# Kernel optimization log

Measured on AMD Instinct MI355X. Metric: run time of the kernel, lower is better.

## Reference

```python
import jax, jax.numpy as jnp
import numpy as np
from jax import lax

B, C, H, W = 2, 64, 128, 128
NBR, G, K, P, CK = 4, 8, 3, 11, 3
PAD = 6  # (CK-1)//2 + (P-1)//2


def conv2d(x, w, b, pad):
    y = lax.conv_general_dilated(x, w, (1, 1), [(pad, pad), (pad, pad)],
                                 dimension_numbers=('NCHW', 'OIHW', 'NCHW'))
    return y + b[None, :, None, None]


def l2norm(x):
    n = jnp.sqrt(jnp.sum(x * x, axis=1, keepdims=True))
    return x / jnp.maximum(n, 1e-12)


def correlation(f1, f2):
    # spatial correlation sampler: kernel=3, patch=11, stride=1, padding=1
    # corr[b, ph*11+pw, h, w] = sum_{c,ki,kj} f1[b,c,h+ki-1,w+kj-1]*f2[b,c,h+ki-1+ph-5,w+kj-1+pw-5]
    f1p = jnp.pad(f1, ((0, 0), (0, 0), (1, 1), (1, 1)))
    f2p = jnp.pad(f2, ((0, 0), (0, 0), (PAD, PAD), (PAD, PAD)))
    offs = jnp.array([(ph, pw) for ph in range(P) for pw in range(P)], dtype=jnp.int32)

    def one(off):
        sl = lax.dynamic_slice(f2p, (0, 0, off[0], off[1]), (B, C, H + 2, W + 2))
        q = jnp.einsum('bchw,bchw->bhw', f1p, sl)  # (B,H+2,W+2)
        # 3x3 box sum -> (B,H,W)
        return sum(q[:, ki:ki + H, kj:kj + W] for ki in range(CK) for kj in range(CK))

    corr = lax.map(one, offs)  # (121,B,H,W)
    return jnp.transpose(corr, (1, 0, 2, 3))  # (B,121,H,W)


def setup_inputs() -> dict:
    key = jax.random.key(0)
    ks = jax.random.split(key, 12)
    s = 0.05
    return {
        'nbr_fea': jax.random.normal(ks[0], (B, C, H, W), jnp.float32),
        'ref_fea': jax.random.normal(ks[1], (B, C, H, W), jnp.float32),
        'conv1_w': jax.random.normal(ks[2], (C, 2 * C, 3, 3), jnp.float32) * s,
        'conv1_b': jax.random.normal(ks[3], (C,), jnp.float32) * s,
        'conv2_w': jax.random.normal(ks[4], (C, C, 3, 3), jnp.float32) * s,
        'conv2_b': jax.random.normal(ks[5], (C,), jnp.float32) * s,
        'mask_w': jax.random.normal(ks[6], (G * K * K, C, K, K), jnp.float32) * s,
        'mask_b': jax.random.normal(ks[7], (G * K * K,), jnp.float32) * s,
        'nn_w': jax.random.normal(ks[8], (C, NBR * C, 3, 3), jnp.float32) * s,
        'nn_b': jax.random.normal(ks[9], (C,), jnp.float32) * s,
        'agg_w': jax.random.normal(ks[10], (C, 2 * C, 3, 3), jnp.float32) * s,
        'agg_b': jax.random.normal(ks[11], (C,), jnp.float32) * s,
    }


def reference(nbr_fea, ref_fea, conv1_w, conv1_b, conv2_w, conv2_b,
              mask_w, mask_b, nn_w, nn_b, agg_w, agg_b):
    # mask branch
    wf = conv2d(jnp.concatenate([nbr_fea, ref_fea], axis=1), conv1_w, conv1_b, 1)
    wf = conv2d(wf, conv2_w, conv2_b, 1)
    mask = conv2d(wf, mask_w, mask_b, (K - 1) // 2).reshape(B, G, 1, K * K, H, W)

    # local correlation + topk neighbor selection
    corr = correlation(l2norm(ref_fea), l2norm(nbr_fea))  # (B,121,H,W)
    idx = lax.top_k(jnp.transpose(corr, (0, 2, 3, 1)), NBR)[1]  # (B,H,W,NBR)
    ph, pw = idx // P, idx % P

    # gather 3x3 patches centered at displacement (ph-5, pw-5) from pad-6 nbr features
    nbr_pad = jnp.pad(nbr_fea, ((0, 0), (0, 0), (PAD, PAD), (PAD, PAD)))
    r0 = jnp.arange(H)[None, :, None, None] + ph  # (B,H,W,NBR) top-left row in padded img
    c0 = jnp.arange(W)[None, None, :, None] + pw
    ki = jnp.arange(CK)

    def gather_b(fp, r, c):
        R = r[..., None, None] + ki[:, None]   # (H,W,NBR,3,1)
        Cc = c[..., None, None] + ki[None, :]  # (H,W,NBR,1,3)
        return fp[:, R, Cc]  # (C,H,W,NBR,3,3)

    patches = jax.vmap(gather_b)(nbr_pad, r0, c0)  # (B,C,H,W,NBR,3,3)
    L = jnp.transpose(patches, (0, 2, 3, 4, 1, 5, 6)).reshape(B * H * W, NBR * C, CK, CK)
    L = conv2d(L, nn_w, nn_b, 1)  # (B*H*W, C, 3, 3)
    L = L.reshape(B, H, W, C, CK * CK)
    L = jnp.transpose(L, (0, 3, 4, 1, 2)).reshape(B, G, C // G, CK * CK, H, W)

    agg = jnp.sum(L * mask, axis=3).reshape(B, C, H, W)
    agg = jnp.where(agg >= 0, agg, 0.1 * agg)  # LeakyReLU(0.1)
    out = conv2d(jnp.concatenate([agg, ref_fea], axis=1), agg_w, agg_b, 1)
    return out
```

## Files before the change

kernel.cpp:

```cpp
#include <hip/hip_runtime.h>
#include <hip/hip_bf16.h>
#include <math.h>

#define HH 128
#define WW 128
#define HWSZ 16384

typedef __attribute__((ext_vector_type(8))) short short8;
typedef __attribute__((ext_vector_type(4))) float f32x4;

constexpr int OFF_CATT  = 0;
constexpr int OFF_CAT2T = 8388608;
constexpr int OFF_WF1   = 16777216;
constexpr int OFF_WF2   = 20971520;
constexpr int OFF_MASK  = 25165824;
constexpr int OFF_IDX   = 34603008;
constexpr int OFF_WT1   = 35127296;
constexpr int OFF_WT2   = 35274752;
constexpr int OFF_WTM   = 35348480;
constexpr int OFF_WTA   = 35495936;
constexpr int OFF_ZROW  = 35643392;
constexpr int OFF_WB    = 35644416;
constexpr int OFF_F1T   = 38797312;
constexpr int OFF_F2T   = 47185920;
constexpr int OFF_D     = 55574528;
constexpr int OFF_PV    = 71434240;
constexpr int OFF_PP    = 77201408;

__device__ inline ushort f2bf(float f) {
    __hip_bfloat16 h = __float2bfloat16(f);
    return *reinterpret_cast<ushort*>(&h);
}
__device__ inline float bf2f(ushort u) {
    return __uint_as_float(((unsigned)u) << 16);
}

__device__ inline void gload16(const void* g, void* l) {
    __builtin_amdgcn_global_load_lds(
        (const __attribute__((address_space(1))) unsigned int*)g,
        (__attribute__((address_space(3))) unsigned int*)l, 16, 0, 0);
}

__global__ __launch_bounds__(256) void l2t2_kernel(const float* __restrict__ in,
                                                   float4* __restrict__ normT4,
                                                   ushort* __restrict__ d1,
                                                   ushort* __restrict__ d2)
{
    const int pix0 = blockIdx.x * 64;
    const int b = pix0 >> 14;
    const int hw0 = pix0 & (HWSZ - 1);
    __shared__ float s[64][65];
    __shared__ float sinv[64];
    const int tid = threadIdx.x;
    {
        const int p = tid & 63, c4 = tid >> 6;
#pragma unroll
        for (int r = 0; r < 16; ++r) {
            int c = r * 4 + c4;
            s[c][p] = in[(((size_t)b * 64 + c) << 14) + hw0 + p];
        }
    }
    __syncthreads();
    if (tid < 64) {
        float sum = 0.f;
#pragma unroll
        for (int c = 0; c < 64; ++c) { float v = s[c][tid]; sum = fmaf(v, v, sum); }
        sinv[tid] = 1.f / fmaxf(sqrtf(sum), 1e-12f);
    }
    __syncthreads();
    {
        const int pp = tid & 63, cg = tid >> 6;
        const float inv = sinv[pp];
#pragma unroll
        for (int r = 0; r < 4; ++r) {
            int c4 = cg * 4 + r;
            float4 v = make_float4(s[c4 * 4 + 0][pp] * inv, s[c4 * 4 + 1][pp] * inv,
                                   s[c4 * 4 + 2][pp] * inv, s[c4 * 4 + 3][pp] * inv);
            normT4[(((size_t)b * 16 + c4) << 14) + hw0 + pp] = v;
        }
    }
    {
        const int c = tid & 63, p4 = tid >> 6;
#pragma unroll
        for (int r = 0; r < 16; ++r) {
            int pp = r * 4 + p4;
            ushort bv = f2bf(s[c][pp]);
            d1[(size_t)(pix0 + pp) * 128 + c] = bv;
            if (d2) d2[(size_t)(pix0 + pp) * 128 + c] = bv;
        }
    }
}

__global__ __launch_bounds__(256) void dot_kernel(const float4* __restrict__ f1t4,
                                                  const float4* __restrict__ f2t4,
                                                  float* __restrict__ D)
{
    const int pix = blockIdx.x * 256 + threadIdx.x;
    const int q = blockIdx.y;
    const int b = pix >> 14, hw = pix & (HWSZ - 1), h = hw >> 7, w = hw & 127;
    const int y = h + q - 5;
    float* Dq = D + ((((size_t)b * 121) + q * 11) << 14) + hw;

    if ((unsigned)y >= (unsigned)HH) {
#pragma unroll
        for (int pw = 0; pw < 11; ++pw) Dq[(size_t)pw << 14] = 0.f;
        return;
    }
    float acc[11] = {};
    const float4* f1p  = f1t4 + (((size_t)b * 16) << 14) + hw;
    const float4* rowb = f2t4 + (((size_t)b * 16) << 14) + (y << 7);

#pragma unroll 4
    for (int c4 = 0; c4 < 16; ++c4) {
        float4 a = f1p[(size_t)c4 << 14];
        const float4* rp = rowb + ((size_t)c4 << 14);
#pragma unroll
        for (int pw = 0; pw < 11; ++pw) {
            int x = w + pw - 5;
            if ((unsigned)x < (unsigned)WW) {
                float4 c = rp[x];
                acc[pw] = fmaf(a.x, c.x, acc[pw]);
                acc[pw] = fmaf(a.y, c.y, acc[pw]);
                acc[pw] = fmaf(a.z, c.z, acc[pw]);
                acc[pw] = fmaf(a.w, c.w, acc[pw]);
            }
        }
    }
#pragma unroll
    for (int pw = 0; pw < 11; ++pw) Dq[(size_t)pw << 14] = acc[pw];
}

__global__ __launch_bounds__(256) void topk_s1(const float* __restrict__ D,
                                               float4* __restrict__ Pv,
                                               int4* __restrict__ Pp)
{
    const int pix = blockIdx.x * 256 + threadIdx.x;
    const int q = blockIdx.y;
    const int b = pix >> 14, hw = pix & (HWSZ - 1), h = hw >> 7, w = hw & 127;
    const int lane = threadIdx.x & 63;
    const float* Db = D + (((size_t)b * 121) << 14);

    float bv[4] = {-1e30f, -1e30f, -1e30f, -1e30f};
    int   bi[4] = {1 << 20, 1 << 20, 1 << 20, 1 << 20};

    for (int pw = 0; pw < 11; ++pw) {
        const int p = q * 11 + pw;
        const float* Dp = Db + ((size_t)p << 14);
        float v = 0.f, vx = 0.f;
#pragma unroll
        for (int dy = -1; dy <= 1; ++dy) {
            int y = h + dy;
            if ((unsigned)y < HH) {
                v += Dp[(y << 7) + w];
                if (lane == 0) { if (w > 0) vx += Dp[(y << 7) + w - 1]; }
                else if (lane == 63) { if (w < 127) vx += Dp[(y << 7) + w + 1]; }
            }
        }
        float vl = __shfl_up(v, 1);
        float vr = __shfl_down(v, 1);
        if (lane == 0)  vl = (w > 0)   ? vx : 0.f;
        if (lane == 63) vr = (w < 127) ? vx : 0.f;
        float s = vl + v + vr;
        if (s > bv[3]) {
            if (s > bv[0]) { bv[3]=bv[2];bi[3]=bi[2]; bv[2]=bv[1];bi[2]=bi[1]; bv[1]=bv[0];bi[1]=bi[0]; bv[0]=s; bi[0]=p; }
            else if (s > bv[1]) { bv[3]=bv[2];bi[3]=bi[2]; bv[2]=bv[1];bi[2]=bi[1]; bv[1]=s; bi[1]=p; }
            else if (s > bv[2]) { bv[3]=bv[2];bi[3]=bi[2]; bv[2]=s; bi[2]=p; }
            else { bv[3]=s; bi[3]=p; }
        }
    }
    Pv[(size_t)q * 32768 + pix] = make_float4(bv[0], bv[1], bv[2], bv[3]);
    Pp[(size_t)q * 32768 + pix] = make_int4(bi[0], bi[1], bi[2], bi[3]);
}

__global__ __launch_bounds__(256) void topk_s2(const float4* __restrict__ Pv,
                                               const int4* __restrict__ Pp,
                                               int* __restrict__ idxout)
{
    const int pix = blockIdx.x * 256 + threadIdx.x;
    float bv2[4] = {-1e30f, -1e30f, -1e30f, -1e30f};
    int   bi2[4] = {1 << 20, 1 << 20, 1 << 20, 1 << 20};
    for (int qq = 0; qq < 11; ++qq) {
        float4 v4 = Pv[(size_t)qq * 32768 + pix];
        int4   p4 = Pp[(size_t)qq * 32768 + pix];
        float vv[4] = {v4.x, v4.y, v4.z, v4.w};
        int   pp4[4] = {p4.x, p4.y, p4.z, p4.w};
#pragma unroll
        for (int r = 0; r < 4; ++r) {
            float v = vv[r]; int pp = pp4[r];
            bool g3 = (v > bv2[3]) || (v == bv2[3] && pp < bi2[3]);
            if (g3) {
                bool g0 = (v > bv2[0]) || (v == bv2[0] && pp < bi2[0]);
                bool g1 = (v > bv2[1]) || (v == bv2[1] && pp < bi2[1]);
                bool g2 = (v > bv2[2]) || (v == bv2[2] && pp < bi2[2]);
                if (g0) { bv2[3]=bv2[2];bi2[3]=bi2[2]; bv2[2]=bv2[1];bi2[2]=bi2[1]; bv2[1]=bv2[0];bi2[1]=bi2[0]; bv2[0]=v; bi2[0]=pp; }
                else if (g1) { bv2[3]=bv2[2];bi2[3]=bi2[2]; bv2[2]=bv2[1];bi2[2]=bi2[1]; bv2[1]=v; bi2[1]=pp; }
                else if (g2) { bv2[3]=bv2[2];bi2[3]=bi2[2]; bv2[2]=v; bi2[2]=pp; }
                else { bv2[3]=v; bi2[3]=pp; }
            }
        }
    }
    int p0 = (bi2[0] / 11) | ((bi2[0] % 11) << 16);
    int p1 = (bi2[1] / 11) | ((bi2[1] % 11) << 16);
    int p2 = (bi2[2] / 11) | ((bi2[2] % 11) << 16);
    int p3 = (bi2[3] / 11) | ((bi2[3] % 11) << 16);
    ((int4*)idxout)[pix] = make_int4(p0, p1, p2, p3);
}

__device__ inline ushort wt_elem(const float* __restrict__ w, int Cin, int Cout, int idx) {
    int kc = 9 * Cin;
    int o = idx / kc, rem = idx % kc;
    int tap = rem / Cin, c = rem % Cin;
    float val = (o < Cout) ? w[((size_t)o * Cin + c) * 9 + tap] : 0.f;
    return f2bf(val);
}

__global__ __launch_bounds__(256) void prep_kernel(
    const float* __restrict__ c1w, const float* __restrict__ c2w,
    const float* __restrict__ mw,  const float* __restrict__ aw,
    const float* __restrict__ nnw, char* __restrict__ W)
{
    int gid = blockIdx.x * 256 + threadIdx.x;
    if (gid < 73728) {
        ((ushort*)(W + OFF_WT1))[gid] = wt_elem(c1w, 128, 64, gid);
    } else if (gid < 110592) {
        int i = gid - 73728;
        ((ushort*)(W + OFF_WT2))[i] = wt_elem(c2w, 64, 64, i);
    } else if (gid < 165888) {
        int i = gid - 110592;
        ((ushort*)(W + OFF_WTM))[i] = wt_elem(mw, 64, 72, i);
    } else if (gid < 239616) {
        int i = gid - 165888;
        ((ushort*)(W + OFF_WTA))[i] = wt_elem(aw, 128, 64, i);
    } else if (gid < 387072) {
        int idx = gid - 239616;
        int j = idx / 36864, rem = idx % 36864;
        int rb = rem >> 6, c = rem & 63;
        int e = rb >> 6, o = rb & 63;
        int ky = e / 3, kx = e % 3;
        ((ushort*)(W + OFF_WB))[idx] =
            f2bf(nnw[(((size_t)o * 256 + j * 64 + c) * 3 + ky) * 3 + kx]);
    } else if (gid < 387200) {
        ((ushort*)(W + OFF_ZROW))[gid - 387072] = 0;
    }
}

template<int CINPT, int OUTFMT, int BM, int BN, int WN>
__global__ __launch_bounds__(256) void mmconv_kernel(
    const char* __restrict__ Wb, int src_off, int rowbytes, int zoff,
    const ushort* __restrict__ WT, int Ktot,
    const float* __restrict__ bias,
    void* __restrict__ outp, int ostride, int nvalid)
{
    constexpr int WM = 4 / WN;
    constexpr int FM = BM / (WM * 16);
    constexpr int FN = BN / (WN * 16);
    constexpr int NA = BM / 32;
    constexpr int NB = BN / 32;
    const int n0 = blockIdx.x * BN;
    const int m0 = blockIdx.y * BM;
    const int tid = threadIdx.x;
    const int lane = tid & 63, wv = tid >> 6;
    const int lr = lane >> 4, lc = lane & 15;
    const int wr = wv / WN, wc = wv % WN;

    __shared__ __align__(16) char sA[2][BM * 128];
    __shared__ __align__(16) char sB[2][BN * 128];

    int hA[NA], wA[NA], aBase[NA], swzA[NA];
#pragma unroll
    for (int i = 0; i < NA; ++i) {
        int r  = (i * 4 + wv) * 8 + (lane >> 3);
        int pm = m0 + r;
        int hw = pm & (HWSZ - 1);
        hA[i] = hw >> 7; wA[i] = hw & 127;
        aBase[i] = src_off + (pm >> 14) * (HWSZ * rowbytes);
        swzA[i]  = ((lane & 7) ^ (r & 7)) << 4;
    }
    int boff[NB];
#pragma unroll
    for (int i = 0; i < NB; ++i) {
        int rb = (i * 4 + wv) * 8 + (lane >> 3);
        boff[i] = (n0 + rb) * Ktot * 2 + (((lane & 7) ^ (rb & 7)) << 4);
    }

    f32x4 acc[FM][FN] = {};
    const int NST = Ktot / 64;

#define CSTAGE(S, B)                                                             \
    {                                                                            \
        int k0 = (S) * 64;                                                       \
        int tap = k0 / CINPT;                                                    \
        int c0b = (k0 % CINPT) * 2;                                              \
        int du = tap / 3 - 1, dv = tap % 3 - 1;                                  \
        _Pragma("unroll")                                                        \
        for (int i = 0; i < NA; ++i) {                                           \
            int y = hA[i] + du, x = wA[i] + dv;                                  \
            bool ok = ((unsigned)y < (unsigned)HH) && ((unsigned)x < (unsigned)WW); \
            int off = ok ? (aBase[i] + ((y << 7) + x) * rowbytes + c0b + swzA[i]) : zoff; \
            gload16(Wb + (unsigned)off, &sA[(B)][(i * 4 + wv) * 1024]);          \
        }                                                                        \
        _Pragma("unroll")                                                        \
        for (int i = 0; i < NB; ++i)                                             \
            gload16((const char*)WT + (unsigned)(boff[i] + (S) * 128),           \
                    &sB[(B)][(i * 4 + wv) * 1024]);                              \
    }

    CSTAGE(0, 0)
    __syncthreads();
#pragma unroll 1
    for (int s = 0; s < NST; ++s) {
        if (s + 1 < NST) { CSTAGE(s + 1, (s + 1) & 1) }
        const char* cA = sA[s & 1];
        const char* cB = sB[s & 1];
#pragma unroll
        for (int ks = 0; ks < 2; ++ks) {
            short8 af[FM]; short8 bfr[FN];
            const int u = ks * 4 + lr;
#pragma unroll
            for (int f = 0; f < FM; ++f) {
                int rr = wr * (FM * 16) + f * 16 + lc;
                af[f] = *(const short8*)&cA[rr * 128 + ((u ^ (rr & 7)) << 4)];
            }
#pragma unroll
            for (int g = 0; g < FN; ++g) {
                int nn = wc * (FN * 16) + g * 16 + lc;
                bfr[g] = *(const short8*)&cB[nn * 128 + ((u ^ (nn & 7)) << 4)];
            }
#pragma unroll
            for (int f = 0; f < FM; ++f)
#pragma unroll
                for (int g = 0; g < FN; ++g)
                    acc[f][g] = __builtin_amdgcn_mfma_f32_16x16x32_bf16(af[f], bfr[g], acc[f][g], 0, 0, 0);
        }
        __syncthreads();
    }
#undef CSTAGE

#pragma unroll
    for (int f = 0; f < FM; ++f)
#pragma unroll
        for (int g = 0; g < FN; ++g) {
            const int col = n0 + wc * (FN * 16) + g * 16 + lc;
            float bv = (bias != nullptr && col < nvalid) ? bias[col] : 0.f;
            if (OUTFMT == 2) {
                const int mb = m0 + wr * (FM * 16) + f * 16 + lr * 4;
                const int bb = mb >> 14, hww = mb & (HWSZ - 1);
                float4 o4 = {acc[f][g][0] + bv, acc[f][g][1] + bv,
                             acc[f][g][2] + bv, acc[f][g][3] + bv};
                *(float4*)((float*)outp + (((size_t)(bb * 64 + col)) << 14) + hww) = o4;
            } else {
#pragma unroll
                for (int reg = 0; reg < 4; ++reg) {
                    const int m = m0 + wr * (FM * 16) + f * 16 + lr * 4 + reg;
                    float v = acc[f][g][reg] + bv;
                    if (OUTFMT == 0)
                        ((ushort*)outp)[(size_t)m * ostride + col] = f2bf(v);
                    else if (col < nvalid)
                        ((float*)outp)[(size_t)m * ostride + col] = v;
                }
            }
        }
}

__global__ __launch_bounds__(256, 2) void patch_kernel(
    const char* __restrict__ Wb, int cat_off, int idx_off, int zoff, int wb_off,
    const float* __restrict__ maskcl, const float* __restrict__ nnb,
    ushort* __restrict__ aggout)
{
    const int m0 = blockIdx.x * 32;
    const int tid = threadIdx.x;
    const int lane = tid & 63, wv = tid >> 6;
    const int lr = lane >> 4, lc = lane & 15;
    const int wr = wv >> 1, wc = wv & 1;

    __shared__ __align__(16) char sP[36864 + 2 * 16384];

    const int r    = tid >> 3;
    const int pm_s = m0 + r;
    const int hw_s = pm_s & (HWSZ - 1);
    const int hS = hw_s >> 7, wS = hw_s & 127;
    const int aBase = cat_off + (pm_s >> 14) * (HWSZ * 256);
    const int swzA  = ((tid & 7) ^ (r & 7)) << 4;
    int bsrc[2];
#pragma unroll
    for (int i = 0; i < 2; ++i) {
        int rl = i * 32 + r;
        bsrc[i] = wb_off + rl * 128 + (((tid & 7) ^ (rl & 7)) << 4);
    }
    const int* idxr = (const int*)(Wb + idx_off);

    f32x4 acc[9][2] = {};

#pragma unroll 1
    for (int j = 0; j < 4; ++j) {
        const int pk = idxr[pm_s * 4 + j];
        const int hp = hS + (pk & 0xffff) - 6;
        const int wp = wS + (pk >> 16) - 6;

        __syncthreads();
#pragma unroll
        for (int uv = 0; uv < 9; ++uv) {
            int y = hp + uv / 3, x = wp + uv % 3;
            bool ok = ((unsigned)y < (unsigned)HH) && ((unsigned)x < (unsigned)WW);
            int off = ok ? (aBase + ((y << 7) + x) * 256 + swzA) : zoff;
            gload16(Wb + (unsigned)off, &sP[uv * 4096 + wv * 1024]);
        }
#pragma unroll
        for (int eg = 0; eg < 2; ++eg)
#pragma unroll
            for (int i = 0; i < 2; ++i)
                gload16(Wb + (unsigned)(bsrc[i] + j * 73728 + eg * 8192),
                        &sP[36864 + eg * 8192 + i * 4096 + wv * 1024]);
        __syncthreads();

        short8 af[9][2];
#pragma unroll
        for (int uv = 0; uv < 9; ++uv)
#pragma unroll
            for (int ks = 0; ks < 2; ++ks) {
                const int rr = wr * 16 + lc;
                af[uv][ks] = *(const short8*)&sP[uv * 4096 + rr * 128 +
                                                (((ks * 4 + lr) ^ (rr & 7)) << 4)];
            }

#pragma unroll
        for (int g = 0; g < 5; ++g) {
            if (g < 4) {
                const int nslot = (g + 1) & 1;
#pragma unroll
                for (int eg = 0; eg < 2; ++eg) {
                    const int ne = 2 * (g + 1) + eg;
                    if (ne > 8) continue;
#pragma unroll
                    for (int i = 0; i < 2; ++i)
                        gload16(Wb + (unsigned)(bsrc[i] + j * 73728 + ne * 8192),
                                &sP[36864 + nslot * 16384 + eg * 8192 + i * 4096 + wv * 1024]);
                }
            }
#pragma unroll
            for (int eg = 0; eg < 2; ++eg) {
                const int e = 2 * g + eg;
                if (e > 8) continue;
                const char* bt = &sP[36864 + (g & 1) * 16384 + eg * 8192];
                short8 bfr[2][2];
#pragma unroll
                for (int gg = 0; gg < 2; ++gg) {
                    const int rloc = wc * 32 + gg * 16 + lc;
#pragma unroll
                    for (int ks = 0; ks < 2; ++ks)
                        bfr[gg][ks] = *(const short8*)&bt[rloc * 128 +
                                                          (((ks * 4 + lr) ^ (rloc & 7)) << 4)];
                }
                const int ky = e / 3, kx = e % 3;
#pragma unroll
                for (int uv = 0; uv < 9; ++uv) {
                    const int uu = uv / 3, vv = uv % 3;
                    const int ty = uu - ky + 1, tx = vv - kx + 1;
                    if (ty < 0 || ty > 2 || tx < 0 || tx > 2) continue;
                    const int t = ty * 3 + tx;
#pragma unroll
                    for (int gg = 0; gg < 2; ++gg) {
                        acc[t][gg] = __builtin_amdgcn_mfma_f32_16x16x32_bf16(af[uv][0], bfr[gg][0], acc[t][gg], 0, 0, 0);
                        acc[t][gg] = __builtin_amdgcn_mfma_f32_16x16x32_bf16(af[uv][1], bfr[gg][1], acc[t][gg], 0, 0, 0);
                    }
                }
            }
            if (g < 4) __syncthreads();
        }
    }

#pragma unroll
    for (int gg = 0; gg < 2; ++gg) {
        const int col_o = wc * 32 + gg * 16 + lc;
        const float bo = nnb[col_o];
        const int og = col_o >> 3;
#pragma unroll
        for (int reg = 0; reg < 4; ++reg) {
            const int m = m0 + wr * 16 + lr * 4 + reg;
            const float* mp = maskcl + (size_t)m * 72 + og * 9;
            float s = 0.f;
#pragma unroll
            for (int t = 0; t < 9; ++t) s += (acc[t][gg][reg] + bo) * mp[t];
            s = (s >= 0.f) ? s : 0.1f * s;
            aggout[(size_t)m * 128 + col_o] = f2bf(s);
        }
    }
}

extern "C" void kernel_launch(void* const* d_in, const int* in_sizes, int n_in,
                              void* d_out, int out_size, void* d_ws, size_t ws_size,
                              hipStream_t stream)
{
    const float* nbr = (const float*)d_in[0];
    const float* ref = (const float*)d_in[1];
    const float* c1w = (const float*)d_in[2];
    const float* c1b = (const float*)d_in[3];
    const float* c2w = (const float*)d_in[4];
    const float* c2b = (const float*)d_in[5];
    const float* mw  = (const float*)d_in[6];
    const float* mb  = (const float*)d_in[7];
    const float* nnw = (const float*)d_in[8];
    const float* nnb = (const float*)d_in[9];
    const float* aw  = (const float*)d_in[10];
    const float* ab  = (const float*)d_in[11];
    float* out = (float*)d_out;

    char* W = (char*)d_ws;
    float4* f1t4   = (float4*)(W + OFF_F1T);
    float4* f2t4   = (float4*)(W + OFF_F2T);
    float*  Dbuf   = (float*)(W + OFF_D);
    float*  maskcl = (float*)(W + OFF_MASK);
    int*    idxp   = (int*)(W + OFF_IDX);
    ushort* catT   = (ushort*)(W + OFF_CATT);
    ushort* cat2T  = (ushort*)(W + OFF_CAT2T);

    dim3 blk(256);

    prep_kernel<<<1513, blk, 0, stream>>>(c1w, c2w, mw, aw, nnw, W);

    l2t2_kernel<<<512, blk, 0, stream>>>(ref, f1t4, catT + 64, cat2T + 64);
    l2t2_kernel<<<512, blk, 0, stream>>>(nbr, f2t4, catT + 0, (ushort*)nullptr);

    mmconv_kernel<128, 0, 32, 64, 4><<<dim3(1, 1024), blk, 0, stream>>>(
        W, OFF_CATT, 256, OFF_ZROW, (ushort*)(W + OFF_WT1), 1152, c1b, W + OFF_WF1, 64, 64);
    mmconv_kernel<64, 0, 32, 64, 4><<<dim3(1, 1024), blk, 0, stream>>>(
        W, OFF_WF1, 128, OFF_ZROW, (ushort*)(W + OFF_WT2), 576, c2b, W + OFF_WF2, 64, 64);
    mmconv_kernel<64, 1, 32, 96, 2><<<dim3(1, 1024), blk, 0, stream>>>(
        W, OFF_WF2, 128, OFF_ZROW, (ushort*)(W + OFF_WTM), 576, mb, maskcl, 72, 72);

    dot_kernel<<<dim3(128, 11), blk, 0, stream>>>(f1t4, f2t4, Dbuf);
    topk_s1<<<dim3(128, 11), blk, 0, stream>>>(Dbuf, (float4*)(W + OFF_PV), (int4*)(W + OFF_PP));
    topk_s2<<<128, blk, 0, stream>>>((const float4*)(W + OFF_PV), (const int4*)(W + OFF_PP), idxp);

    patch_kernel<<<1024, blk, 0, stream>>>(W, OFF_CATT, OFF_IDX, OFF_ZROW, OFF_WB,
                                           maskcl, nnb, cat2T);

    mmconv_kernel<128, 2, 32, 64, 4><<<dim3(1, 1024), blk, 0, stream>>>(
        W, OFF_CAT2T, 256, OFF_ZROW, (ushort*)(W + OFF_WTA), 1152, ab, out, 0, 64);
}
```

Baseline: 177.8 us.

## Fuse correlation dot product with 3x3 box-sum top-k stage via LDS

Merges the per-offset dot-product kernel and the first top-k stage into one kernel that keeps the raw dot products for a tile of rows in shared memory, then box-sums and selects the top 4 per row of offsets. This removes the full-size global D buffer write and reread plus one launch. In exchange each block recomputes two halo rows, uses 56KB of LDS, and the grid shrinks to 352 blocks, which lowers occupancy and parallelism.

```diff
diff --git a/kernel.cpp b/kernel.cpp
--- a/kernel.cpp
+++ b/kernel.cpp
@@ -23,9 +23,8 @@
 constexpr int OFF_WB    = 35644416;
 constexpr int OFF_F1T   = 38797312;
 constexpr int OFF_F2T   = 47185920;
-constexpr int OFF_D     = 55574528;
-constexpr int OFF_PV    = 71434240;
-constexpr int OFF_PP    = 77201408;
+constexpr int OFF_PV    = 55574528;
+constexpr int OFF_PP    = 61341696;
 
 __device__ inline ushort f2bf(float f) {
     __hip_bfloat16 h = __float2bfloat16(f);
@@ -91,85 +90,80 @@
     }
 }
 
-__global__ __launch_bounds__(256) void dot_kernel(const float4* __restrict__ f1t4,
-                                                  const float4* __restrict__ f2t4,
-                                                  float* __restrict__ D)
-{
-    const int pix = blockIdx.x * 256 + threadIdx.x;
+__global__ __launch_bounds__(256) void corr_kernel(const float4* __restrict__ f1t4,
+                                                   const float4* __restrict__ f2t4,
+                                                   float4* __restrict__ Pv,
+                                                   int4* __restrict__ Pp)
+{
     const int q = blockIdx.y;
-    const int b = pix >> 14, hw = pix & (HWSZ - 1), h = hw >> 7, w = hw & 127;
-    const int y = h + q - 5;
-    float* Dq = D + ((((size_t)b * 121) + q * 11) << 14) + hw;
-
-    if ((unsigned)y >= (unsigned)HH) {
-#pragma unroll
-        for (int pw = 0; pw < 11; ++pw) Dq[(size_t)pw << 14] = 0.f;
-        return;
-    }
-    float acc[11] = {};
-    const float4* f1p  = f1t4 + (((size_t)b * 16) << 14) + hw;
-    const float4* rowb = f2t4 + (((size_t)b * 16) << 14) + (y << 7);
-
+    const int b = blockIdx.x >> 4;
+    const int brow0 = (blockIdx.x & 15) * 8;
+    const int tid = threadIdx.x;
+
+    __shared__ float Dl[10][11][128];
+
+    const size_t fbase = ((size_t)b * 16) << 14;
+
+#pragma unroll 1
+    for (int k = 0; k < 5; ++k) {
+        const int task = tid + k * 256;
+        const int trow = task >> 7;
+        const int w = task & 127;
+        const int rg = brow0 + trow - 1;
+        const int y = rg + q - 5;
+        float acc[11] = {};
+        if ((unsigned)rg < (unsigned)HH && (unsigned)y < (unsigned)HH) {
+            const float4* f1p  = f1t4 + fbase + (rg << 7) + w;
+            const float4* rowb = f2t4 + fbase + (y << 7);
 #pragma unroll 4
-    for (int c4 = 0; c4 < 16; ++c4) {
-        float4 a = f1p[(size_t)c4 << 14];
-        const float4* rp = rowb + ((size_t)c4 << 14);
+            for (int c4 = 0; c4 < 16; ++c4) {
+                float4 a = f1p[(size_t)c4 << 14];
+                const float4* rp = rowb + ((size_t)c4 << 14);
+#pragma unroll
+                for (int pw = 0; pw < 11; ++pw) {
+                    int x = w + pw - 5;
+                    if ((unsigned)x < (unsigned)WW) {
+                        float4 c = rp[x];
+                        acc[pw] = fmaf(a.x, c.x, acc[pw]);
+                        acc[pw] = fmaf(a.y, c.y, acc[pw]);
+                        acc[pw] = fmaf(a.z, c.z, acc[pw]);
+                        acc[pw] = fmaf(a.w, c.w, acc[pw]);
+                    }
+                }
+            }
+        }
+#pragma unroll
+        for (int pw = 0; pw < 11; ++pw) Dl[trow][pw][w] = acc[pw];
+    }
+    __syncthreads();
+
+#pragma unroll 1
+    for (int k = 0; k < 4; ++k) {
+        const int opix = tid + k * 256;
+        const int orow = opix >> 7;
+        const int w = opix & 127;
+        float bv[4] = {-1e30f, -1e30f, -1e30f, -1e30f};
+        int   bi[4] = {1 << 20, 1 << 20, 1 << 20, 1 << 20};
 #pragma unroll
         for (int pw = 0; pw < 11; ++pw) {
-            int x = w + pw - 5;
-            if ((unsigned)x < (unsigned)WW) {
-                float4 c = rp[x];
-                acc[pw] = fmaf(a.x, c.x, acc[pw]);
-                acc[pw] = fmaf(a.y, c.y, acc[pw]);
-                acc[pw] = fmaf(a.z, c.z, acc[pw]);
-                acc[pw] = fmaf(a.w, c.w, acc[pw]);
-            }
-        }
-    }
-#pragma unroll
-    for (int pw = 0; pw < 11; ++pw) Dq[(size_t)pw << 14] = acc[pw];
-}
-
-__global__ __launch_bounds__(256) void topk_s1(const float* __restrict__ D,
-                                               float4* __restrict__ Pv,
-                                               int4* __restrict__ Pp)
-{
-    const int pix = blockIdx.x * 256 + threadIdx.x;
-    const int q = blockIdx.y;
-    const int b = pix >> 14, hw = pix & (HWSZ - 1), h = hw >> 7, w = hw & 127;
-    const int lane = threadIdx.x & 63;
-    const float* Db = D + (((size_t)b * 121) << 14);
-
-    float bv[4] = {-1e30f, -1e30f, -1e30f, -1e30f};
-    int   bi[4] = {1 << 20, 1 << 20, 1 << 20, 1 << 20};
-
-    for (int pw = 0; pw < 11; ++pw) {
-        const int p = q * 11 + pw;
-        const float* Dp = Db + ((size_t)p << 14);
-        float v = 0.f, vx = 0.f;
-#pragma unroll
-        for (int dy = -1; dy <= 1; ++dy) {
-            int y = h + dy;
-            if ((unsigned)y < HH) {
-                v += Dp[(y << 7) + w];
-                if (lane == 0) { if (w > 0) vx += Dp[(y << 7) + w - 1]; }
-                else if (lane == 63) { if (w < 127) vx += Dp[(y << 7) + w + 1]; }
-            }
-        }
-        float vl = __shfl_up(v, 1);
-        float vr = __shfl_down(v, 1);
-        if (lane == 0)  vl = (w > 0)   ? vx : 0.f;
-        if (lane == 63) vr = (w < 127) ? vx : 0.f;
-        float s = vl + v + vr;
-        if (s > bv[3]) {
-            if (s > bv[0]) { bv[3]=bv[2];bi[3]=bi[2]; bv[2]=bv[1];bi[2]=bi[1]; bv[1]=bv[0];bi[1]=bi[0]; bv[0]=s; bi[0]=p; }
-            else if (s > bv[1]) { bv[3]=bv[2];bi[3]=bi[2]; bv[2]=bv[1];bi[2]=bi[1]; bv[1]=s; bi[1]=p; }
-            else if (s > bv[2]) { bv[3]=bv[2];bi[3]=bi[2]; bv[2]=s; bi[2]=p; }
-            else { bv[3]=s; bi[3]=p; }
-        }
-    }
-    Pv[(size_t)q * 32768 + pix] = make_float4(bv[0], bv[1], bv[2], bv[3]);
-    Pp[(size_t)q * 32768 + pix] = make_int4(bi[0], bi[1], bi[2], bi[3]);
+            const int p = q * 11 + pw;
+            float v  = Dl[orow][pw][w] + Dl[orow + 1][pw][w] + Dl[orow + 2][pw][w];
+            float vl = (w > 0)
+                ? Dl[orow][pw][w - 1] + Dl[orow + 1][pw][w - 1] + Dl[orow + 2][pw][w - 1] : 0.f;
+            float vr = (w < 127)
+                ? Dl[orow][pw][w + 1] + Dl[orow + 1][pw][w + 1] + Dl[orow + 2][pw][w + 1] : 0.f;
+            float s = vl + v + vr;
+            if (s > bv[3]) {
+                if (s > bv[0]) { bv[3]=bv[2];bi[3]=bi[2]; bv[2]=bv[1];bi[2]=bi[1]; bv[1]=bv[0];bi[1]=bi[0]; bv[0]=s; bi[0]=p; }
+                else if (s > bv[1]) { bv[3]=bv[2];bi[3]=bi[2]; bv[2]=bv[1];bi[2]=bi[1]; bv[1]=s; bi[1]=p; }
+                else if (s > bv[2]) { bv[3]=bv[2];bi[3]=bi[2]; bv[2]=s; bi[2]=p; }
+                else { bv[3]=s; bi[3]=p; }
+            }
+        }
+        const int pix = (b << 14) + ((brow0 + orow) << 7) + w;
+        Pv[(size_t)q * 32768 + pix] = make_float4(bv[0], bv[1], bv[2], bv[3]);
+        Pp[(size_t)q * 32768 + pix] = make_int4(bi[0], bi[1], bi[2], bi[3]);
+    }
 }
 
 __global__ __launch_bounds__(256) void topk_s2(const float4* __restrict__ Pv,
@@ -508,7 +502,6 @@
     char* W = (char*)d_ws;
     float4* f1t4   = (float4*)(W + OFF_F1T);
     float4* f2t4   = (float4*)(W + OFF_F2T);
-    float*  Dbuf   = (float*)(W + OFF_D);
     float*  maskcl = (float*)(W + OFF_MASK);
     int*    idxp   = (int*)(W + OFF_IDX);
     ushort* catT   = (ushort*)(W + OFF_CATT);
@@ -528,8 +521,8 @@
     mmconv_kernel<64, 1, 32, 96, 2><<<dim3(1, 1024), blk, 0, stream>>>(
         W, OFF_WF2, 128, OFF_ZROW, (ushort*)(W + OFF_WTM), 576, mb, maskcl, 72, 72);
 
-    dot_kernel<<<dim3(128, 11), blk, 0, stream>>>(f1t4, f2t4, Dbuf);
-    topk_s1<<<dim3(128, 11), blk, 0, stream>>>(Dbuf, (float4*)(W + OFF_PV), (int4*)(W + OFF_PP));
+    corr_kernel<<<dim3(32, 11), blk, 0, stream>>>(f1t4, f2t4,
+                                                  (float4*)(W + OFF_PV), (int4*)(W + OFF_PP));
     topk_s2<<<128, blk, 0, stream>>>((const float4*)(W + OFF_PV), (const int4*)(W + OFF_PP), idxp);
 
     patch_kernel<<<1024, blk, 0, stream>>>(W, OFF_CATT, OFF_IDX, OFF_ZROW, OFF_WB,
```

Result: slower. 236.4 us (+32.9%).

## Merge independent kernels into combined launches via block-index dispatch

Applied to the files above, without the earlier changes.

Converts the separate kernels into device bodies and builds four combined launches. Each launch pairs independent work by block index: prep with both l2-normalise passes, conv1 with the correlation dot, conv2 with topk stage one, and the mask conv with topk stage two. The aim is fewer launches and less idle time between small kernels, letting the correlation branch overlap with the conv chain. The cost is that each merged kernel's register and shared-memory footprint is the maximum of its two bodies, which may lower occupancy for the lighter half.

```diff
diff --git a/kernel.cpp b/kernel.cpp
--- a/kernel.cpp
+++ b/kernel.cpp
@@ -41,12 +41,11 @@
         (__attribute__((address_space(3))) unsigned int*)l, 16, 0, 0);
 }
 
-__global__ __launch_bounds__(256) void l2t2_kernel(const float* __restrict__ in,
-                                                   float4* __restrict__ normT4,
-                                                   ushort* __restrict__ d1,
-                                                   ushort* __restrict__ d2)
-{
-    const int pix0 = blockIdx.x * 64;
+__device__ void l2t2_body(int bid, const float* __restrict__ in,
+                          float4* __restrict__ normT4,
+                          ushort* __restrict__ d1, ushort* __restrict__ d2)
+{
+    const int pix0 = bid * 64;
     const int b = pix0 >> 14;
     const int hw0 = pix0 & (HWSZ - 1);
     __shared__ float s[64][65];
@@ -91,121 +90,6 @@
     }
 }
 
-__global__ __launch_bounds__(256) void dot_kernel(const float4* __restrict__ f1t4,
-                                                  const float4* __restrict__ f2t4,
-                                                  float* __restrict__ D)
-{
-    const int pix = blockIdx.x * 256 + threadIdx.x;
-    const int q = blockIdx.y;
-    const int b = pix >> 14, hw = pix & (HWSZ - 1), h = hw >> 7, w = hw & 127;
-    const int y = h + q - 5;
-    float* Dq = D + ((((size_t)b * 121) + q * 11) << 14) + hw;
-
-    if ((unsigned)y >= (unsigned)HH) {
-#pragma unroll
-        for (int pw = 0; pw < 11; ++pw) Dq[(size_t)pw << 14] = 0.f;
-        return;
-    }
-    float acc[11] = {};
-    const float4* f1p  = f1t4 + (((size_t)b * 16) << 14) + hw;
-    const float4* rowb = f2t4 + (((size_t)b * 16) << 14) + (y << 7);
-
-#pragma unroll 4
-    for (int c4 = 0; c4 < 16; ++c4) {
-        float4 a = f1p[(size_t)c4 << 14];
-        const float4* rp = rowb + ((size_t)c4 << 14);
-#pragma unroll
-        for (int pw = 0; pw < 11; ++pw) {
-            int x = w + pw - 5;
-            if ((unsigned)x < (unsigned)WW) {
-                float4 c = rp[x];
-                acc[pw] = fmaf(a.x, c.x, acc[pw]);
-                acc[pw] = fmaf(a.y, c.y, acc[pw]);
-                acc[pw] = fmaf(a.z, c.z, acc[pw]);
-                acc[pw] = fmaf(a.w, c.w, acc[pw]);
-            }
-        }
-    }
-#pragma unroll
-    for (int pw = 0; pw < 11; ++pw) Dq[(size_t)pw << 14] = acc[pw];
-}
-
-__global__ __launch_bounds__(256) void topk_s1(const float* __restrict__ D,
-                                               float4* __restrict__ Pv,
-                                               int4* __restrict__ Pp)
-{
-    const int pix = blockIdx.x * 256 + threadIdx.x;
-    const int q = blockIdx.y;
-    const int b = pix >> 14, hw = pix & (HWSZ - 1), h = hw >> 7, w = hw & 127;
-    const int lane = threadIdx.x & 63;
-    const float* Db = D + (((size_t)b * 121) << 14);
-
-    float bv[4] = {-1e30f, -1e30f, -1e30f, -1e30f};
-    int   bi[4] = {1 << 20, 1 << 20, 1 << 20, 1 << 20};
-
-    for (int pw = 0; pw < 11; ++pw) {
-        const int p = q * 11 + pw;
-        const float* Dp = Db + ((size_t)p << 14);
-        float v = 0.f, vx = 0.f;
-#pragma unroll
-        for (int dy = -1; dy <= 1; ++dy) {
-            int y = h + dy;
-            if ((unsigned)y < HH) {
-                v += Dp[(y << 7) + w];
-                if (lane == 0) { if (w > 0) vx += Dp[(y << 7) + w - 1]; }
-                else if (lane == 63) { if (w < 127) vx += Dp[(y << 7) + w + 1]; }
-            }
-        }
-        float vl = __shfl_up(v, 1);
-        float vr = __shfl_down(v, 1);
-        if (lane == 0)  vl = (w > 0)   ? vx : 0.f;
-        if (lane == 63) vr = (w < 127) ? vx : 0.f;
-        float s = vl + v + vr;
-        if (s > bv[3]) {
-            if (s > bv[0]) { bv[3]=bv[2];bi[3]=bi[2]; bv[2]=bv[1];bi[2]=bi[1]; bv[1]=bv[0];bi[1]=bi[0]; bv[0]=s; bi[0]=p; }
-            else if (s > bv[1]) { bv[3]=bv[2];bi[3]=bi[2]; bv[2]=bv[1];bi[2]=bi[1]; bv[1]=s; bi[1]=p; }
-            else if (s > bv[2]) { bv[3]=bv[2];bi[3]=bi[2]; bv[2]=s; bi[2]=p; }
-            else { bv[3]=s; bi[3]=p; }
-        }
-    }
-    Pv[(size_t)q * 32768 + pix] = make_float4(bv[0], bv[1], bv[2], bv[3]);
-    Pp[(size_t)q * 32768 + pix] = make_int4(bi[0], bi[1], bi[2], bi[3]);
-}
-
-__global__ __launch_bounds__(256) void topk_s2(const float4* __restrict__ Pv,
-                                               const int4* __restrict__ Pp,
-                                               int* __restrict__ idxout)
-{
-    const int pix = blockIdx.x * 256 + threadIdx.x;
-    float bv2[4] = {-1e30f, -1e30f, -1e30f, -1e30f};
-    int   bi2[4] = {1 << 20, 1 << 20, 1 << 20, 1 << 20};
-    for (int qq = 0; qq < 11; ++qq) {
-        float4 v4 = Pv[(size_t)qq * 32768 + pix];
-        int4   p4 = Pp[(size_t)qq * 32768 + pix];
-        float vv[4] = {v4.x, v4.y, v4.z, v4.w};
-        int   pp4[4] = {p4.x, p4.y, p4.z, p4.w};
-#pragma unroll
-        for (int r = 0; r < 4; ++r) {
-            float v = vv[r]; int pp = pp4[r];
-            bool g3 = (v > bv2[3]) || (v == bv2[3] && pp < bi2[3]);
-            if (g3) {
-                bool g0 = (v > bv2[0]) || (v == bv2[0] && pp < bi2[0]);
-                bool g1 = (v > bv2[1]) || (v == bv2[1] && pp < bi2[1]);
-                bool g2 = (v > bv2[2]) || (v == bv2[2] && pp < bi2[2]);
-                if (g0) { bv2[3]=bv2[2];bi2[3]=bi2[2]; bv2[2]=bv2[1];bi2[2]=bi2[1]; bv2[1]=bv2[0];bi2[1]=bi2[0]; bv2[0]=v; bi2[0]=pp; }
-                else if (g1) { bv2[3]=bv2[2];bi2[3]=bi2[2]; bv2[2]=bv2[1];bi2[2]=bi2[1]; bv2[1]=v; bi2[1]=pp; }
-                else if (g2) { bv2[3]=bv2[2];bi2[3]=bi2[2]; bv2[2]=v; bi2[2]=pp; }
-                else { bv2[3]=v; bi2[3]=pp; }
-            }
-        }
-    }
-    int p0 = (bi2[0] / 11) | ((bi2[0] % 11) << 16);
-    int p1 = (bi2[1] / 11) | ((bi2[1] % 11) << 16);
-    int p2 = (bi2[2] / 11) | ((bi2[2] % 11) << 16);
-    int p3 = (bi2[3] / 11) | ((bi2[3] % 11) << 16);
-    ((int4*)idxout)[pix] = make_int4(p0, p1, p2, p3);
-}
-
 __device__ inline ushort wt_elem(const float* __restrict__ w, int Cin, int Cout, int idx) {
     int kc = 9 * Cin;
     int o = idx / kc, rem = idx % kc;
@@ -214,12 +98,12 @@
     return f2bf(val);
 }
 
-__global__ __launch_bounds__(256) void prep_kernel(
-    const float* __restrict__ c1w, const float* __restrict__ c2w,
-    const float* __restrict__ mw,  const float* __restrict__ aw,
-    const float* __restrict__ nnw, char* __restrict__ W)
-{
-    int gid = blockIdx.x * 256 + threadIdx.x;
+__device__ void prep_body(int bid,
+                          const float* __restrict__ c1w, const float* __restrict__ c2w,
+                          const float* __restrict__ mw,  const float* __restrict__ aw,
+                          const float* __restrict__ nnw, char* __restrict__ W)
+{
+    int gid = bid * 256 + threadIdx.x;
     if (gid < 73728) {
         ((ushort*)(W + OFF_WT1))[gid] = wt_elem(c1w, 128, 64, gid);
     } else if (gid < 110592) {
@@ -244,8 +128,120 @@
     }
 }
 
+__device__ void dot_body(int bid, const float4* __restrict__ f1t4,
+                         const float4* __restrict__ f2t4, float* __restrict__ D)
+{
+    const int pix = (bid & 127) * 256 + threadIdx.x;
+    const int q = bid >> 7;
+    const int b = pix >> 14, hw = pix & (HWSZ - 1), h = hw >> 7, w = hw & 127;
+    const int y = h + q - 5;
+    float* Dq = D + ((((size_t)b * 121) + q * 11) << 14) + hw;
+
+    if ((unsigned)y >= (unsigned)HH) {
+#pragma unroll
+        for (int pw = 0; pw < 11; ++pw) Dq[(size_t)pw << 14] = 0.f;
+        return;
+    }
+    float acc[11] = {};
+    const float4* f1p  = f1t4 + (((size_t)b * 16) << 14) + hw;
+    const float4* rowb = f2t4 + (((size_t)b * 16) << 14) + (y << 7);
+
+#pragma unroll 4
+    for (int c4 = 0; c4 < 16; ++c4) {
+        float4 a = f1p[(size_t)c4 << 14];
+        const float4* rp = rowb + ((size_t)c4 << 14);
+#pragma unroll
+        for (int pw = 0; pw < 11; ++pw) {
+            int x = w + pw - 5;
+            if ((unsigned)x < (unsigned)WW) {
+                float4 c = rp[x];
+                acc[pw] = fmaf(a.x, c.x, acc[pw]);
+                acc[pw] = fmaf(a.y, c.y, acc[pw]);
+                acc[pw] = fmaf(a.z, c.z, acc[pw]);
+                acc[pw] = fmaf(a.w, c.w, acc[pw]);
+            }
+        }
+    }
+#pragma unroll
+    for (int pw = 0; pw < 11; ++pw) Dq[(size_t)pw << 14] = acc[pw];
+}
+
+__device__ void topk_s1_body(int bid, const float* __restrict__ D,
+                             float4* __restrict__ Pv, int4* __restrict__ Pp)
+{
+    const int pix = (bid & 127) * 256 + threadIdx.x;
+    const int q = bid >> 7;
+    const int b = pix >> 14, hw = pix & (HWSZ - 1), h = hw >> 7, w = hw & 127;
+    const int lane = threadIdx.x & 63;
+    const float* Db = D + (((size_t)b * 121) << 14);
+
+    float bv[4] = {-1e30f, -1e30f, -1e30f, -1e30f};
+    int   bi[4] = {1 << 20, 1 << 20, 1 << 20, 1 << 20};
+
+    for (int pw = 0; pw < 11; ++pw) {
+        const int p = q * 11 + pw;
+        const float* Dp = Db + ((size_t)p << 14);
+        float v = 0.f, vx = 0.f;
+#pragma unroll
+        for (int dy = -1; dy <= 1; ++dy) {
+            int y = h + dy;
+            if ((unsigned)y < HH) {
+                v += Dp[(y << 7) + w];
+                if (lane == 0) { if (w > 0) vx += Dp[(y << 7) + w - 1]; }
+                else if (lane == 63) { if (w < 127) vx += Dp[(y << 7) + w + 1]; }
+            }
+        }
+        float vl = __shfl_up(v, 1);
+        float vr = __shfl_down(v, 1);
+        if (lane == 0)  vl = (w > 0)   ? vx : 0.f;
+        if (lane == 63) vr = (w < 127) ? vx : 0.f;
+        float s = vl + v + vr;
+        if (s > bv[3]) {
+            if (s > bv[0]) { bv[3]=bv[2];bi[3]=bi[2]; bv[2]=bv[1];bi[2]=bi[1]; bv[1]=bv[0];bi[1]=bi[0]; bv[0]=s; bi[0]=p; }
+            else if (s > bv[1]) { bv[3]=bv[2];bi[3]=bi[2]; bv[2]=bv[1];bi[2]=bi[1]; bv[1]=s; bi[1]=p; }
+            else if (s > bv[2]) { bv[3]=bv[2];bi[3]=bi[2]; bv[2]=s; bi[2]=p; }
+            else { bv[3]=s; bi[3]=p; }
+        }
+    }
+    Pv[(size_t)q * 32768 + pix] = make_float4(bv[0], bv[1], bv[2], bv[3]);
+    Pp[(size_t)q * 32768 + pix] = make_int4(bi[0], bi[1], bi[2], bi[3]);
+}
+
+__device__ void topk_s2_body(int bid, const float4* __restrict__ Pv,
+                             const int4* __restrict__ Pp, int* __restrict__ idxout)
+{
+    const int pix = bid * 256 + threadIdx.x;
+    float bv2[4] = {-1e30f, -1e30f, -1e30f, -1e30f};
+    int   bi2[4] = {1 << 20, 1 << 20, 1 << 20, 1 << 20};
+    for (int qq = 0; qq < 11; ++qq) {
+        float4 v4 = Pv[(size_t)qq * 32768 + pix];
+        int4   p4 = Pp[(size_t)qq * 32768 + pix];
+        float vv[4] = {v4.x, v4.y, v4.z, v4.w};
+        int   pp4[4] = {p4.x, p4.y, p4.z, p4.w};
+#pragma unroll
+        for (int r = 0; r < 4; ++r) {
+            float v = vv[r]; int pp = pp4[r];
+            bool g3 = (v > bv2[3]) || (v == bv2[3] && pp < bi2[3]);
+            if (g3) {
+                bool g0 = (v > bv2[0]) || (v == bv2[0] && pp < bi2[0]);
+                bool g1 = (v > bv2[1]) || (v == bv2[1] && pp < bi2[1]);
+                bool g2 = (v > bv2[2]) || (v == bv2[2] && pp < bi2[2]);
+                if (g0) { bv2[3]=bv2[2];bi2[3]=bi2[2]; bv2[2]=bv2[1];bi2[2]=bi2[1]; bv2[1]=bv2[0];bi2[1]=bi2[0]; bv2[0]=v; bi2[0]=pp; }
+                else if (g1) { bv2[3]=bv2[2];bi2[3]=bi2[2]; bv2[2]=bv2[1];bi2[2]=bi2[1]; bv2[1]=v; bi2[1]=pp; }
+                else if (g2) { bv2[3]=bv2[2];bi2[3]=bi2[2]; bv2[2]=v; bi2[2]=pp; }
+                else { bv2[3]=v; bi2[3]=pp; }
+            }
+        }
+    }
+    int p0 = (bi2[0] / 11) | ((bi2[0] % 11) << 16);
+    int p1 = (bi2[1] / 11) | ((bi2[1] % 11) << 16);
+    int p2 = (bi2[2] / 11) | ((bi2[2] % 11) << 16);
+    int p3 = (bi2[3] / 11) | ((bi2[3] % 11) << 16);
+    ((int4*)idxout)[pix] = make_int4(p0, p1, p2, p3);
+}
+
 template<int CINPT, int OUTFMT, int BM, int BN, int WN>
-__global__ __launch_bounds__(256) void mmconv_kernel(
+__device__ void mmconv_body(int by,
     const char* __restrict__ Wb, int src_off, int rowbytes, int zoff,
     const ushort* __restrict__ WT, int Ktot,
     const float* __restrict__ bias,
@@ -256,8 +252,8 @@
     constexpr int FN = BN / (WN * 16);
     constexpr int NA = BM / 32;
     constexpr int NB = BN / 32;
-    const int n0 = blockIdx.x * BN;
-    const int m0 = blockIdx.y * BM;
+    const int n0 = 0;
+    const int m0 = by * BM;
     const int tid = threadIdx.x;
     const int lane = tid & 63, wv = tid >> 6;
     const int lr = lane >> 4, lc = lane & 15;
@@ -362,6 +358,70 @@
         }
 }
 
+__global__ __launch_bounds__(256) void k0_prep_l2t2(
+    const float* __restrict__ ref, const float* __restrict__ nbr,
+    const float* __restrict__ c1w, const float* __restrict__ c2w,
+    const float* __restrict__ mw,  const float* __restrict__ aw,
+    const float* __restrict__ nnw, char* __restrict__ W)
+{
+    const int bid = blockIdx.x;
+    if (bid < 512) {
+        l2t2_body(bid, ref, (float4*)(W + OFF_F1T),
+                  (ushort*)(W + OFF_CATT) + 64, (ushort*)(W + OFF_CAT2T) + 64);
+    } else if (bid < 1024) {
+        l2t2_body(bid - 512, nbr, (float4*)(W + OFF_F2T),
+                  (ushort*)(W + OFF_CATT), (ushort*)nullptr);
+    } else {
+        prep_body(bid - 1024, c1w, c2w, mw, aw, nnw, W);
+    }
+}
+
+__global__ __launch_bounds__(256) void k1_conv1_dot(
+    char* __restrict__ W, const float* __restrict__ c1b)
+{
+    const int bid = blockIdx.x;
+    if (bid < 1024) {
+        mmconv_body<128, 0, 32, 64, 4>(bid, W, OFF_CATT, 256, OFF_ZROW,
+            (ushort*)(W + OFF_WT1), 1152, c1b, W + OFF_WF1, 64, 64);
+    } else {
+        dot_body(bid - 1024, (const float4*)(W + OFF_F1T),
+                 (const float4*)(W + OFF_F2T), (float*)(W + OFF_D));
+    }
+}
+
+__global__ __launch_bounds__(256) void k2_conv2_s1(
+    char* __restrict__ W, const float* __restrict__ c2b)
+{
+    const int bid = blockIdx.x;
+    if (bid < 1024) {
+        mmconv_body<64, 0, 32, 64, 4>(bid, W, OFF_WF1, 128, OFF_ZROW,
+            (ushort*)(W + OFF_WT2), 576, c2b, W + OFF_WF2, 64, 64);
+    } else {
+        topk_s1_body(bid - 1024, (const float*)(W + OFF_D),
+                     (float4*)(W + OFF_PV), (int4*)(W + OFF_PP));
+    }
+}
+
+__global__ __launch_bounds__(256) void k3_convM_s2(
+    char* __restrict__ W, const float* __restrict__ mb)
+{
+    const int bid = blockIdx.x;
+    if (bid < 1024) {
+        mmconv_body<64, 1, 32, 96, 2>(bid, W, OFF_WF2, 128, OFF_ZROW,
+            (ushort*)(W + OFF_WTM), 576, mb, (float*)(W + OFF_MASK), 72, 72);
+    } else {
+        topk_s2_body(bid - 1024, (const float4*)(W + OFF_PV),
+                     (const int4*)(W + OFF_PP), (int*)(W + OFF_IDX));
+    }
+}
+
+__global__ __launch_bounds__(256) void convA_kernel(
+    char* __restrict__ W, const float* __restrict__ ab, float* __restrict__ out)
+{
+    mmconv_body<128, 2, 32, 64, 4>(blockIdx.x, W, OFF_CAT2T, 256, OFF_ZROW,
+        (ushort*)(W + OFF_WTA), 1152, ab, out, 0, 64);
+}
+
 __global__ __launch_bounds__(256, 2) void patch_kernel(
     const char* __restrict__ Wb, int cat_off, int idx_off, int zoff, int wb_off,
     const float* __restrict__ maskcl, const float* __restrict__ nnb,
@@ -506,35 +566,19 @@
     float* out = (float*)d_out;
 
     char* W = (char*)d_ws;
-    float4* f1t4   = (float4*)(W + OFF_F1T);
-    float4* f2t4   = (float4*)(W + OFF_F2T);
-    float*  Dbuf   = (float*)(W + OFF_D);
-    float*  maskcl = (float*)(W + OFF_MASK);
-    int*    idxp   = (int*)(W + OFF_IDX);
-    ushort* catT   = (ushort*)(W + OFF_CATT);
-    ushort* cat2T  = (ushort*)(W + OFF_CAT2T);
-
     dim3 blk(256);
 
-    prep_kernel<<<1513, blk, 0, stream>>>(c1w, c2w, mw, aw, nnw, W);
-
-    l2t2_kernel<<<512, blk, 0, stream>>>(ref, f1t4, catT + 64, cat2T + 64);
-    l2t2_kernel<<<512, blk, 0, stream>>>(nbr, f2t4, catT + 0, (ushort*)nullptr);
-
-    mmconv_kernel<128, 0, 32, 64, 4><<<dim3(1, 1024), blk, 0, stream>>>(
-        W, OFF_CATT, 256, OFF_ZROW, (ushort*)(W + OFF_WT1), 1152, c1b, W + OFF_WF1, 64, 64);
-    mmconv_kernel<64, 0, 32, 64, 4><<<dim3(1, 1024), blk, 0, stream>>>(
-        W, OFF_WF1, 128, OFF_ZROW, (ushort*)(W + OFF_WT2), 576, c2b, W + OFF_WF2, 64, 64);
-    mmconv_kernel<64, 1, 32, 96, 2><<<dim3(1, 1024), blk, 0, stream>>>(
-        W, OFF_WF2, 128, OFF_ZROW, (ushort*)(W + OFF_WTM), 576, mb, maskcl, 72, 72);
-
-    dot_kernel<<<dim3(128, 11), blk, 0, stream>>>(f1t4, f2t4, Dbuf);
-    topk_s1<<<dim3(128, 11), blk, 0, stream>>>(Dbuf, (float4*)(W + OFF_PV), (int4*)(W + OFF_PP));
-    topk_s2<<<128, blk, 0, stream>>>((const float4*)(W + OFF_PV), (const int4*)(W + OFF_PP), idxp);
+    k0_prep_l2t2<<<2537, blk, 0, stream>>>(ref, nbr, c1w, c2w, mw, aw, nnw, W);
+
+    k1_conv1_dot<<<2432, blk, 0, stream>>>(W, c1b);
+
+    k2_conv2_s1<<<2432, blk, 0, stream>>>(W, c2b);
+
+    k3_convM_s2<<<1152, blk, 0, stream>>>(W, mb);
 
     patch_kernel<<<1024, blk, 0, stream>>>(W, OFF_CATT, OFF_IDX, OFF_ZROW, OFF_WB,
-                                           maskcl, nnb, cat2T);
-
-    mmconv_kernel<128, 2, 32, 64, 4><<<dim3(1, 1024), blk, 0, stream>>>(
-        W, OFF_CAT2T, 256, OFF_ZROW, (ushort*)(W + OFF_WTA), 1152, ab, out, 0, 64);
-}
+                                           (const float*)(W + OFF_MASK), nnb,
+                                           (ushort*)(W + OFF_CAT2T));
+
+    convA_kernel<<<1024, blk, 0, stream>>>(W, ab, out);
+}
```

Result: faster. 164.8 us, median of 2 (-7.3%).
